# Kernel tuning notes

Measured on AMD Instinct MI355X. Metric: run time of the kernel, lower is better.

## Reference

```python
import jax, jax.numpy as jnp
import numpy as np

N, E, F, C = 50000, 640000, 128, 128  # nodes, edges, in_feat, hidden_channels
NEG_SLOPE = 0.2  # PyG GATConv default negative_slope


def setup_inputs() -> dict:
    key = jax.random.key(0)
    ks = jax.random.split(key, 16)
    s_in = 1.0 / np.sqrt(F)
    s_hid = 1.0 / np.sqrt(C)
    inp = {
        'x': jax.random.normal(ks[0], (N, F), jnp.float32),
        'edge_index': jax.random.randint(ks[1], (2, E), 0, N),
        # layer 1: GATConv (lin_src, lin_dst, att_src, att_dst, bias) + skip Linear
        'W1s': jax.random.normal(ks[2], (F, C), jnp.float32) * s_in,
        'W1d': jax.random.normal(ks[3], (F, C), jnp.float32) * s_in,
        'a1s': jax.random.normal(ks[4], (C,), jnp.float32) * s_hid,
        'a1d': jax.random.normal(ks[5], (C,), jnp.float32) * s_hid,
        'b1': jnp.zeros((C,), jnp.float32),
        'Wl1': jax.random.normal(ks[6], (F, C), jnp.float32) * s_in,
        'bl1': jnp.zeros((C,), jnp.float32),
        # layer 2
        'W2s': jax.random.normal(ks[7], (C, C), jnp.float32) * s_hid,
        'W2d': jax.random.normal(ks[8], (C, C), jnp.float32) * s_hid,
        'a2s': jax.random.normal(ks[9], (C,), jnp.float32) * s_hid,
        'a2d': jax.random.normal(ks[10], (C,), jnp.float32) * s_hid,
        'b2': jnp.zeros((C,), jnp.float32),
        'Wl2': jax.random.normal(ks[11], (C, C), jnp.float32) * s_hid,
        'bl2': jnp.zeros((C,), jnp.float32),
    }
    return inp


def gat_conv(x, Ws, Wd, a_s, a_d, b, src, dst):
    # project once per node, not per edge
    h_src = x @ Ws                      # [N, C]
    h_dst = x @ Wd                      # [N, C]
    alpha_src = h_src @ a_s             # [N]
    alpha_dst = h_dst @ a_d             # [N]
    # attention logits on edges: LeakyReLU(a_src[j] + a_dst[i]) for edge j->i
    e = jax.nn.leaky_relu(alpha_src[src] + alpha_dst[dst], NEG_SLOPE)  # [E]
    # segment softmax over incoming edges of each destination node
    e_max = jax.ops.segment_max(e, dst, num_segments=N)                # [N]
    e_exp = jnp.exp(e - e_max[dst])                                    # [E]
    e_sum = jax.ops.segment_sum(e_exp, dst, num_segments=N)            # [N]
    alpha = e_exp / (e_sum[dst] + 1e-16)                               # [E]
    # weighted message gather + scatter-add aggregation
    out = jax.ops.segment_sum(h_src[src] * alpha[:, None], dst, num_segments=N)  # [N, C]
    return out + b


def reference(x, edge_index, W1s, W1d, a1s, a1d, b1, Wl1, bl1,
              W2s, W2d, a2s, a2d, b2, Wl2, bl2):
    src, dst = edge_index[0], edge_index[1]
    h = gat_conv(x, W1s, W1d, a1s, a1d, b1, src, dst) + x @ Wl1 + bl1
    h = jax.nn.relu(h)
    out = gat_conv(h, W2s, W2d, a2s, a2d, b2, src, dst) + h @ Wl2 + bl2
    return out
```

## Files before the change

### kernel.cpp

```cpp
#include <hip/hip_runtime.h>


#define NEG_SLOPE 0.2f
#define SCAN_T 256
#define SCAN_ELE 1024

typedef __attribute__((ext_vector_type(8))) short short8;
typedef __attribute__((ext_vector_type(4))) float f32x4;

__device__ __forceinline__ unsigned short f2bf(float f) {
  unsigned u = __float_as_uint(f);
  u += 0x7FFF + ((u >> 16) & 1);
  return (unsigned short)(u >> 16);
}
__device__ __forceinline__ float bflo(unsigned v) { return __uint_as_float(v << 16); }
__device__ __forceinline__ float bfhi(unsigned v) { return __uint_as_float(v & 0xFFFF0000u); }

__global__ __launch_bounds__(256) void zero_kernel(int* __restrict__ p, int n) {
  int i = blockIdx.x * 256 + threadIdx.x;
  if (i < n) p[i] = 0;
}

__global__ __launch_bounds__(256) void count_kernel(const int* __restrict__ dst,
                                                    int* __restrict__ deg, int E) {
  int e = (blockIdx.x * 256 + threadIdx.x) * 2;
  if (e + 1 < E) {
    int2 d = *(const int2*)(dst + e);
    atomicAdd(&deg[d.x], 1);
    atomicAdd(&deg[d.y], 1);
  } else if (e < E) {
    atomicAdd(&deg[dst[e]], 1);
  }
}

__global__ __launch_bounds__(SCAN_T) void scan_pre(const int* __restrict__ deg,
                                                   int* __restrict__ bsum, int n) {
  __shared__ int red[SCAN_T];
  int b = blockIdx.x, t = threadIdx.x;
  int base = b * SCAN_ELE + t * 4;
  int s = 0;
#pragma unroll
  for (int j = 0; j < 4; ++j) {
    int i = base + j;
    if (i < n) s += deg[i];
  }
  red[t] = s;
  __syncthreads();
  for (int d = SCAN_T / 2; d > 0; d >>= 1) {
    if (t < d) red[t] += red[t + d];
    __syncthreads();
  }
  if (t == 0) bsum[b] = red[0];
}

__global__ __launch_bounds__(256) void scan_mid(const int* __restrict__ bsum,
                                                int* __restrict__ boff,
                                                int* __restrict__ off, int nb, int n) {
  __shared__ int sh[256];
  int t = threadIdx.x;
  int v = (t < nb) ? bsum[t] : 0;
  sh[t] = v;
  __syncthreads();
  for (int d = 1; d < 256; d <<= 1) {
    int u = (t >= d) ? sh[t - d] : 0;
    __syncthreads();
    sh[t] += u;
    __syncthreads();
  }
  if (t < nb) boff[t] = (t == 0) ? 0 : sh[t - 1];
  if (t == 255) off[n] = sh[255];
}

__global__ __launch_bounds__(SCAN_T) void scan_post(const int* __restrict__ deg,
                                                    const int* __restrict__ boff,
                                                    int* __restrict__ off,
                                                    int* __restrict__ cursor, int n) {
  __shared__ int tsum[SCAN_T];
  int b = blockIdx.x, t = threadIdx.x;
  int base = b * SCAN_ELE + t * 4;
  int v[4];
  int s = 0;
#pragma unroll
  for (int j = 0; j < 4; ++j) {
    int i = base + j;
    v[j] = (i < n) ? deg[i] : 0;
    s += v[j];
  }
  tsum[t] = s;
  __syncthreads();
  for (int d = 1; d < SCAN_T; d <<= 1) {
    int u = (t >= d) ? tsum[t - d] : 0;
    __syncthreads();
    tsum[t] += u;
    __syncthreads();
  }
  int run = boff[b] + ((t == 0) ? 0 : tsum[t - 1]);
#pragma unroll
  for (int j = 0; j < 4; ++j) {
    int i = base + j;
    if (i < n) {
      off[i] = run;
      cursor[i] = run;
      run += v[j];
    }
  }
}

__global__ __launch_bounds__(256) void scatter_kernel(const int* __restrict__ src,
                                                      const int* __restrict__ dst,
                                                      int* __restrict__ cursor,
                                                      int* __restrict__ ssorted, int E) {
  int e = (blockIdx.x * 256 + threadIdx.x) * 2;
  if (e + 1 < E) {
    int2 s = *(const int2*)(src + e);
    int2 d = *(const int2*)(dst + e);
    int p0 = atomicAdd(&cursor[d.x], 1);
    ssorted[p0] = s.x;
    int p1 = atomicAdd(&cursor[d.y], 1);
    ssorted[p1] = s.y;
  } else if (e < E) {
    int d = dst[e];
    int pos = atomicAdd(&cursor[d], 1);
    ssorted[pos] = src[e];
  }
}

__global__ __launch_bounds__(256) void wtrans_all(
    const float* __restrict__ W1s, const float* __restrict__ Wl1,
    const float* __restrict__ W2s, const float* __restrict__ Wl2,
    const float* __restrict__ a1s, const float* __restrict__ a1d,
    const float* __restrict__ a2s, const float* __restrict__ a2d,
    const float* __restrict__ W1d, const float* __restrict__ W2d,
    unsigned short* __restrict__ Wt, float* __restrict__ wv) {
  if (blockIdx.x < 256) {
    int idx = blockIdx.x * 256 + threadIdx.x;
    int which = idx >> 14;
    int j = idx & 16383;
    const float* W = (which == 0) ? W1s : (which == 1) ? Wl1 : (which == 2) ? W2s : Wl2;
    int k = j >> 7, c = j & 127;
    Wt[which * 16384 + c * 128 + k] = f2bf(W[k * 128 + c]);
  } else {
    for (int rep = 0; rep < 2; ++rep) {
      int item = threadIdx.x + rep * 256;
      int which = item >> 7, f = item & 127;
      const float* W;
      const float* a;
      if (which == 0)      { W = W1s; a = a1s; }
      else if (which == 1) { W = W1d; a = a1d; }
      else if (which == 2) { W = W2s; a = a2s; }
      else                 { W = W2d; a = a2d; }
      float s = 0.f;
#pragma unroll 8
      for (int c = 0; c < 128; ++c) s += W[f * 128 + c] * a[c];
      wv[which * 128 + f] = s;
    }
  }
}

__global__ __launch_bounds__(256) void prep1(const float* __restrict__ X,
                                             const float* __restrict__ wv,
                                             unsigned short* __restrict__ Xb,
                                             float* __restrict__ asrc,
                                             float* __restrict__ adst, int n) {
  int lane = threadIdx.x & 63;
  int wid = threadIdx.x >> 6;
  int node = blockIdx.x * 4 + wid;
  if (node >= n) return;
  float2 xv = ((const float2*)X)[(size_t)node * 64 + lane];
  float2 sv = ((const float2*)wv)[lane];
  float2 dv = ((const float2*)(wv + 128))[lane];
  unsigned pack = (unsigned)f2bf(xv.x) | ((unsigned)f2bf(xv.y) << 16);
  ((unsigned*)Xb)[(size_t)node * 64 + lane] = pack;
  float ds = xv.x * sv.x + xv.y * sv.y;
  float dd = xv.x * dv.x + xv.y * dv.y;
#pragma unroll
  for (int o = 32; o > 0; o >>= 1) {
    ds += __shfl_down(ds, o);
    dd += __shfl_down(dd, o);
  }
  if (lane == 0) {
    asrc[node] = ds;
    adst[node] = dd;
  }
}

#define SWZ(row, e) ((e) ^ (((row) & 7) << 3))

__global__ __launch_bounds__(256) void gemm_mfma(const unsigned short* __restrict__ Xb,
                                                 const unsigned short* __restrict__ WtA,
                                                 const unsigned short* __restrict__ WtB,
                                                 const float* __restrict__ biasb,
                                                 unsigned short* __restrict__ hsrc,
                                                 float* __restrict__ skip, int n) {
  __shared__ unsigned short sX[64 * 128];
  __shared__ unsigned short sW[128 * 128];
  int y = blockIdx.y;
  const unsigned short* Wt = (y == 0) ? WtA : WtB;
  int r0 = blockIdx.x * 64;
  int tid = threadIdx.x;

#pragma unroll
  for (int cch = 0; cch < 4; ++cch) {
    int id = tid + cch * 256;
    int r = id >> 4;
    int e = (id & 15) * 8;
    int gr = r0 + r;
    short8 v = (short8){0, 0, 0, 0, 0, 0, 0, 0};
    if (gr < n) v = *(const short8*)(Xb + (size_t)gr * 128 + e);
    *(short8*)&sX[r * 128 + SWZ(r, e)] = v;
  }
#pragma unroll
  for (int cch = 0; cch < 8; ++cch) {
    int id = tid + cch * 256;
    int r = id >> 4;
    int e = (id & 15) * 8;
    short8 v = *(const short8*)(Wt + r * 128 + e);
    *(short8*)&sW[r * 128 + SWZ(r, e)] = v;
  }
  __syncthreads();

  int w = tid >> 6, l = tid & 63;
  int q = l >> 4, fr = l & 15;
  int arow = w * 16 + fr;

  short8 af[4];
#pragma unroll
  for (int ks = 0; ks < 4; ++ks)
    af[ks] = *(short8*)&sX[arow * 128 + SWZ(arow, ks * 32 + q * 8)];

  f32x4 acc[8];
#pragma unroll
  for (int ct = 0; ct < 8; ++ct) acc[ct] = (f32x4){0.f, 0.f, 0.f, 0.f};

#pragma unroll
  for (int ct = 0; ct < 8; ++ct) {
    int brow = ct * 16 + fr;
#pragma unroll
    for (int ks = 0; ks < 4; ++ks) {
      short8 bf = *(short8*)&sW[brow * 128 + SWZ(brow, ks * 32 + q * 8)];
      acc[ct] = __builtin_amdgcn_mfma_f32_16x16x32_bf16(af[ks], bf, acc[ct], 0, 0, 0);
    }
  }

  if (y == 0) {
#pragma unroll
    for (int ct = 0; ct < 8; ++ct) {
#pragma unroll
      for (int i = 0; i < 4; ++i) {
        int grow = r0 + w * 16 + q * 4 + i;
        if (grow < n) hsrc[(size_t)grow * 128 + ct * 16 + fr] = f2bf(acc[ct][i]);
      }
    }
  } else {
#pragma unroll
    for (int ct = 0; ct < 8; ++ct) {
      float bv = biasb[ct * 16 + fr];
#pragma unroll
      for (int i = 0; i < 4; ++i) {
        int grow = r0 + w * 16 + q * 4 + i;
        if (grow < n) skip[(size_t)grow * 128 + ct * 16 + fr] = acc[ct][i] + bv;
      }
    }
  }
}

__global__ __launch_bounds__(256) void agg_fused(const int* __restrict__ off,
                                                 const int* __restrict__ ssorted,
                                                 const float* __restrict__ asrc,
                                                 const float* __restrict__ adst,
                                                 const unsigned short* __restrict__ hs,
                                                 const float* __restrict__ skip,
                                                 const float* __restrict__ bias,
                                                 float* __restrict__ outp,
                                                 unsigned short* __restrict__ xb,
                                                 const float* __restrict__ wv2,
                                                 float* __restrict__ asrc2,
                                                 float* __restrict__ adst2,
                                                 int relu, int n) {
  __shared__ float2 s_ae[4][66];
  int lane = threadIdx.x & 63;
  int wid = threadIdx.x >> 6;
  int i = blockIdx.x * 4 + wid;
  if (i >= n) return;
  int s0 = off[i], s1 = off[i + 1];
  float ad = adst[i];
  int half = lane >> 5;
  int cl = lane & 31;

  float a0x = 0.f, a0y = 0.f, a0z = 0.f, a0w = 0.f;
  float a1x = 0.f, a1y = 0.f, a1z = 0.f, a1w = 0.f;
  float psum = 0.f;
  for (int cb = s0; cb < s1; cb += 64) {
    int m = min(64, s1 - cb);
    if (lane < m) {
      int sv = ssorted[cb + lane];
      float e = asrc[sv] + ad;
      e = (e > 0.f) ? e : NEG_SLOPE * e;
      float a = __expf(e);
      psum += a;
      s_ae[wid][lane] = make_float2(a, __int_as_float(sv));
    }
    if (lane == 0 && (m & 1)) s_ae[wid][m] = make_float2(0.f, __int_as_float(0));
    int npair = (m + 1) >> 1;
    int t = 0;
    for (; t + 2 <= npair; t += 2) {
      float2 p0 = s_ae[wid][2 * t + half];
      float2 p1 = s_ae[wid][2 * t + 2 + half];
      uint2 v0 = *(const uint2*)(hs + (size_t)__float_as_int(p0.y) * 128 + cl * 4);
      uint2 v1 = *(const uint2*)(hs + (size_t)__float_as_int(p1.y) * 128 + cl * 4);
      a0x += p0.x * bflo(v0.x); a0y += p0.x * bfhi(v0.x);
      a0z += p0.x * bflo(v0.y); a0w += p0.x * bfhi(v0.y);
      a1x += p1.x * bflo(v1.x); a1y += p1.x * bfhi(v1.x);
      a1z += p1.x * bflo(v1.y); a1w += p1.x * bfhi(v1.y);
    }
    if (t < npair) {
      float2 p0 = s_ae[wid][2 * t + half];
      uint2 v0 = *(const uint2*)(hs + (size_t)__float_as_int(p0.y) * 128 + cl * 4);
      a0x += p0.x * bflo(v0.x); a0y += p0.x * bfhi(v0.x);
      a0z += p0.x * bflo(v0.y); a0w += p0.x * bfhi(v0.y);
    }
  }
#pragma unroll
  for (int o = 32; o > 0; o >>= 1) psum += __shfl_xor(psum, o);
  float inv = 1.f / (psum + 1e-16f);

  float cx = a0x + a1x, cy = a0y + a1y, cz = a0z + a1z, cw = a0w + a1w;
  cx += __shfl_xor(cx, 32);
  cy += __shfl_xor(cy, 32);
  cz += __shfl_xor(cz, 32);
  cw += __shfl_xor(cw, 32);

  float v0 = 0.f, v1 = 0.f, v2 = 0.f, v3 = 0.f;
  if (half == 0) {
    float4 sk = ((const float4*)skip)[(size_t)i * 32 + cl];
    float4 bv = ((const float4*)bias)[cl];
    v0 = cx * inv + bv.x + sk.x;
    v1 = cy * inv + bv.y + sk.y;
    v2 = cz * inv + bv.z + sk.z;
    v3 = cw * inv + bv.w + sk.w;
    if (relu) {
      v0 = fmaxf(v0, 0.f); v1 = fmaxf(v1, 0.f);
      v2 = fmaxf(v2, 0.f); v3 = fmaxf(v3, 0.f);
    }
    if (outp) {
      float4 vo; vo.x = v0; vo.y = v1; vo.z = v2; vo.w = v3;
      ((float4*)outp)[(size_t)i * 32 + cl] = vo;
    }
    if (xb) {
      uint2 pack;
      pack.x = (unsigned)f2bf(v0) | ((unsigned)f2bf(v1) << 16);
      pack.y = (unsigned)f2bf(v2) | ((unsigned)f2bf(v3) << 16);
      ((uint2*)xb)[(size_t)i * 32 + cl] = pack;
    }
  }
  if (xb) {
    float ds = 0.f, dd = 0.f;
    if (half == 0) {
      float4 sv2 = ((const float4*)wv2)[cl];
      float4 dv2 = ((const float4*)(wv2 + 128))[cl];
      ds = v0 * sv2.x + v1 * sv2.y + v2 * sv2.z + v3 * sv2.w;
      dd = v0 * dv2.x + v1 * dv2.y + v2 * dv2.z + v3 * dv2.w;
    }
#pragma unroll
    for (int o = 32; o > 0; o >>= 1) {
      ds += __shfl_xor(ds, o);
      dd += __shfl_xor(dd, o);
    }
    if (lane == 0) {
      asrc2[i] = ds;
      adst2[i] = dd;
    }
  }
}

extern "C" void kernel_launch(void* const* d_in, const int* in_sizes, int n_in,
                              void* d_out, int out_size, void* d_ws, size_t ws_size,
                              hipStream_t stream) {
  const float* x   = (const float*)d_in[0];
  const int*   ei  = (const int*)d_in[1];
  const float* W1s = (const float*)d_in[2];
  const float* W1d = (const float*)d_in[3];
  const float* a1s = (const float*)d_in[4];
  const float* a1d = (const float*)d_in[5];
  const float* b1  = (const float*)d_in[6];
  const float* Wl1 = (const float*)d_in[7];
  const float* bl1 = (const float*)d_in[8];
  const float* W2s = (const float*)d_in[9];
  const float* W2d = (const float*)d_in[10];
  const float* a2s = (const float*)d_in[11];
  const float* a2d = (const float*)d_in[12];
  const float* b2  = (const float*)d_in[13];
  const float* Wl2 = (const float*)d_in[14];
  const float* bl2 = (const float*)d_in[15];

  const int N = in_sizes[0] / 128;
  const int E = in_sizes[1] / 2;
  const int* srcp = ei;
  const int* dstp = ei + E;

  char* base = (char*)d_ws;
  size_t o = 0;
  auto alloc = [&](size_t bytes) -> void* {
    void* p = base + o;
    o += (bytes + 255) & ~(size_t)255;
    return p;
  };
  const int NB = (N + SCAN_ELE - 1) / SCAN_ELE;
  int*   deg     = (int*)alloc((size_t)N * 4);
  int*   off     = (int*)alloc((size_t)(N + 1) * 4);
  int*   cursor  = (int*)alloc((size_t)N * 4);
  int*   bsum    = (int*)alloc((size_t)NB * 4);
  int*   boff    = (int*)alloc((size_t)NB * 4);
  int*   ssorted = (int*)alloc((size_t)E * 4);
  float* asrcA   = (float*)alloc((size_t)N * 4);
  float* adstA   = (float*)alloc((size_t)N * 4);
  float* asrcB   = (float*)alloc((size_t)N * 4);
  float* adstB   = (float*)alloc((size_t)N * 4);
  float* wv      = (float*)alloc(4 * 128 * 4);
  unsigned short* Xb    = (unsigned short*)alloc((size_t)N * 128 * 2);
  unsigned short* Wt    = (unsigned short*)alloc(4 * 128 * 128 * 2);
  unsigned short* hsrcB = (unsigned short*)alloc((size_t)N * 128 * 2);
  float* skip    = (float*)alloc((size_t)N * 128 * 4);
  (void)ws_size; (void)n_in; (void)out_size;

  zero_kernel<<<(N + 255) / 256, 256, 0, stream>>>(deg, N);
  count_kernel<<<(E / 2 + 255) / 256, 256, 0, stream>>>(dstp, deg, E);
  scan_pre<<<NB, SCAN_T, 0, stream>>>(deg, bsum, N);
  scan_mid<<<1, 256, 0, stream>>>(bsum, boff, off, NB, N);
  scan_post<<<NB, SCAN_T, 0, stream>>>(deg, boff, off, cursor, N);
  scatter_kernel<<<(E / 2 + 255) / 256, 256, 0, stream>>>(srcp, dstp, cursor, ssorted, E);
  wtrans_all<<<257, 256, 0, stream>>>(W1s, Wl1, W2s, Wl2, a1s, a1d, a2s, a2d,
                                      W1d, W2d, Wt, wv);

  dim3 ggrid((N + 63) / 64, 2);
  int nwb = (N + 3) / 4;

  prep1<<<nwb, 256, 0, stream>>>(x, wv, Xb, asrcA, adstA, N);
  gemm_mfma<<<ggrid, 256, 0, stream>>>(Xb, Wt, Wt + 16384, bl1, hsrcB, skip, N);
  agg_fused<<<nwb, 256, 0, stream>>>(off, ssorted, asrcA, adstA, hsrcB, skip, b1,
                                     nullptr, Xb, wv + 256, asrcB, adstB, 1, N);

  gemm_mfma<<<ggrid, 256, 0, stream>>>(Xb, Wt + 2 * 16384, Wt + 3 * 16384, bl2,
                                       hsrcB, skip, N);
  agg_fused<<<nwb, 256, 0, stream>>>(off, ssorted, asrcB, adstB, hsrcB, skip, b2,
                                     (float*)d_out, nullptr, nullptr, nullptr,
                                     nullptr, 0, N);
}
```

Baseline: 316.0 us.

## Fuse input prep into GEMM and compute both projections per block

Removes the prep1 kernel. The layer-1 GEMM now reads fp32 x directly, converts it to bf16 in-kernel and computes the attention dot products with shuffles. The GEMM grid drops its y-dimension, so each block reuses its loaded X tile for both the source and skip projections, reloading the weight tile in between. The edge count and scatter kernels process four edges per thread with int4 loads, and the weight transpose swaps its k/c index mapping so writes are contiguous. Fewer blocks in the GEMM grid lowers parallelism, and the second weight load adds an extra barrier.

Result: faster. 307.1 us (-2.8%).

```diff
diff --git a/kernel.cpp b/kernel.cpp
--- a/kernel.cpp
+++ b/kernel.cpp
@@ -23,13 +23,15 @@
 
 __global__ __launch_bounds__(256) void count_kernel(const int* __restrict__ dst,
                                                     int* __restrict__ deg, int E) {
-  int e = (blockIdx.x * 256 + threadIdx.x) * 2;
-  if (e + 1 < E) {
-    int2 d = *(const int2*)(dst + e);
+  int e = (blockIdx.x * 256 + threadIdx.x) * 4;
+  if (e + 3 < E) {
+    int4 d = *(const int4*)(dst + e);
     atomicAdd(&deg[d.x], 1);
     atomicAdd(&deg[d.y], 1);
-  } else if (e < E) {
-    atomicAdd(&deg[dst[e]], 1);
+    atomicAdd(&deg[d.z], 1);
+    atomicAdd(&deg[d.w], 1);
+  } else {
+    for (int k = e; k < E; ++k) atomicAdd(&deg[dst[k]], 1);
   }
 }
 
@@ -110,18 +112,16 @@
                                                       const int* __restrict__ dst,
                                                       int* __restrict__ cursor,
                                                       int* __restrict__ ssorted, int E) {
-  int e = (blockIdx.x * 256 + threadIdx.x) * 2;
-  if (e + 1 < E) {
-    int2 s = *(const int2*)(src + e);
-    int2 d = *(const int2*)(dst + e);
-    int p0 = atomicAdd(&cursor[d.x], 1);
-    ssorted[p0] = s.x;
-    int p1 = atomicAdd(&cursor[d.y], 1);
-    ssorted[p1] = s.y;
-  } else if (e < E) {
-    int d = dst[e];
-    int pos = atomicAdd(&cursor[d], 1);
-    ssorted[pos] = src[e];
+  int e = (blockIdx.x * 256 + threadIdx.x) * 4;
+  if (e + 3 < E) {
+    int4 s = *(const int4*)(src + e);
+    int4 d = *(const int4*)(dst + e);
+    ssorted[atomicAdd(&cursor[d.x], 1)] = s.x;
+    ssorted[atomicAdd(&cursor[d.y], 1)] = s.y;
+    ssorted[atomicAdd(&cursor[d.z], 1)] = s.z;
+    ssorted[atomicAdd(&cursor[d.w], 1)] = s.w;
+  } else {
+    for (int k = e; k < E; ++k) ssorted[atomicAdd(&cursor[dst[k]], 1)] = src[k];
   }
 }
 
@@ -137,7 +137,7 @@
     int which = idx >> 14;
     int j = idx & 16383;
     const float* W = (which == 0) ? W1s : (which == 1) ? Wl1 : (which == 2) ? W2s : Wl2;
-    int k = j >> 7, c = j & 127;
+    int c = j >> 7, k = j & 127;
     Wt[which * 16384 + c * 128 + k] = f2bf(W[k * 128 + c]);
   } else {
     for (int rep = 0; rep < 2; ++rep) {
@@ -157,45 +157,17 @@
   }
 }
 
-__global__ __launch_bounds__(256) void prep1(const float* __restrict__ X,
-                                             const float* __restrict__ wv,
-                                             unsigned short* __restrict__ Xb,
-                                             float* __restrict__ asrc,
-                                             float* __restrict__ adst, int n) {
-  int lane = threadIdx.x & 63;
-  int wid = threadIdx.x >> 6;
-  int node = blockIdx.x * 4 + wid;
-  if (node >= n) return;
-  float2 xv = ((const float2*)X)[(size_t)node * 64 + lane];
-  float2 sv = ((const float2*)wv)[lane];
-  float2 dv = ((const float2*)(wv + 128))[lane];
-  unsigned pack = (unsigned)f2bf(xv.x) | ((unsigned)f2bf(xv.y) << 16);
-  ((unsigned*)Xb)[(size_t)node * 64 + lane] = pack;
-  float ds = xv.x * sv.x + xv.y * sv.y;
-  float dd = xv.x * dv.x + xv.y * dv.y;
-#pragma unroll
-  for (int o = 32; o > 0; o >>= 1) {
-    ds += __shfl_down(ds, o);
-    dd += __shfl_down(dd, o);
-  }
-  if (lane == 0) {
-    asrc[node] = ds;
-    adst[node] = dd;
-  }
-}
-
 #define SWZ(row, e) ((e) ^ (((row) & 7) << 3))
 
-__global__ __launch_bounds__(256) void gemm_mfma(const unsigned short* __restrict__ Xb,
-                                                 const unsigned short* __restrict__ WtA,
-                                                 const unsigned short* __restrict__ WtB,
-                                                 const float* __restrict__ biasb,
-                                                 unsigned short* __restrict__ hsrc,
-                                                 float* __restrict__ skip, int n) {
+template <int L1>
+__global__ __launch_bounds__(256) void gemm_mfma(
+    const void* __restrict__ srcX, const unsigned short* __restrict__ WtA,
+    const unsigned short* __restrict__ WtB, const float* __restrict__ biasb,
+    const float* __restrict__ wvsd, unsigned short* __restrict__ hsrc,
+    float* __restrict__ skip, float* __restrict__ asrc, float* __restrict__ adst,
+    int n) {
   __shared__ unsigned short sX[64 * 128];
   __shared__ unsigned short sW[128 * 128];
-  int y = blockIdx.y;
-  const unsigned short* Wt = (y == 0) ? WtA : WtB;
   int r0 = blockIdx.x * 64;
   int tid = threadIdx.x;
 
@@ -203,19 +175,51 @@
   for (int cch = 0; cch < 4; ++cch) {
     int id = tid + cch * 256;
     int r = id >> 4;
-    int e = (id & 15) * 8;
+    int e8 = (id & 15) * 8;
     int gr = r0 + r;
     short8 v = (short8){0, 0, 0, 0, 0, 0, 0, 0};
-    if (gr < n) v = *(const short8*)(Xb + (size_t)gr * 128 + e);
-    *(short8*)&sX[r * 128 + SWZ(r, e)] = v;
-  }
+    float ds = 0.f, dd = 0.f;
+    if (gr < n) {
+      if (L1) {
+        const float* xr = (const float*)srcX + (size_t)gr * 128 + e8;
+        float4 f0 = *(const float4*)xr;
+        float4 f1 = *(const float4*)(xr + 4);
+        v[0] = (short)f2bf(f0.x); v[1] = (short)f2bf(f0.y);
+        v[2] = (short)f2bf(f0.z); v[3] = (short)f2bf(f0.w);
+        v[4] = (short)f2bf(f1.x); v[5] = (short)f2bf(f1.y);
+        v[6] = (short)f2bf(f1.z); v[7] = (short)f2bf(f1.w);
+        float4 s0 = *(const float4*)(wvsd + e8);
+        float4 s1 = *(const float4*)(wvsd + e8 + 4);
+        float4 d0 = *(const float4*)(wvsd + 128 + e8);
+        float4 d1 = *(const float4*)(wvsd + 128 + e8 + 4);
+        ds = f0.x * s0.x + f0.y * s0.y + f0.z * s0.z + f0.w * s0.w +
+             f1.x * s1.x + f1.y * s1.y + f1.z * s1.z + f1.w * s1.w;
+        dd = f0.x * d0.x + f0.y * d0.y + f0.z * d0.z + f0.w * d0.w +
+             f1.x * d1.x + f1.y * d1.y + f1.z * d1.z + f1.w * d1.w;
+      } else {
+        v = *(const short8*)((const unsigned short*)srcX + (size_t)gr * 128 + e8);
+      }
+    }
+    *(short8*)&sX[r * 128 + SWZ(r, e8)] = v;
+    if (L1) {
+#pragma unroll
+      for (int o = 8; o > 0; o >>= 1) {
+        ds += __shfl_down(ds, o);
+        dd += __shfl_down(dd, o);
+      }
+      if ((tid & 15) == 0 && gr < n) {
+        asrc[gr] = ds;
+        adst[gr] = dd;
+      }
+    }
+  }
+
 #pragma unroll
   for (int cch = 0; cch < 8; ++cch) {
     int id = tid + cch * 256;
-    int r = id >> 4;
-    int e = (id & 15) * 8;
-    short8 v = *(const short8*)(Wt + r * 128 + e);
-    *(short8*)&sW[r * 128 + SWZ(r, e)] = v;
+    int rr = id >> 4;
+    int ee = (id & 15) * 8;
+    *(short8*)&sW[rr * 128 + SWZ(rr, ee)] = *(const short8*)(WtA + rr * 128 + ee);
   }
   __syncthreads();
 
@@ -231,7 +235,6 @@
   f32x4 acc[8];
 #pragma unroll
   for (int ct = 0; ct < 8; ++ct) acc[ct] = (f32x4){0.f, 0.f, 0.f, 0.f};
-
 #pragma unroll
   for (int ct = 0; ct < 8; ++ct) {
     int brow = ct * 16 + fr;
@@ -241,25 +244,43 @@
       acc[ct] = __builtin_amdgcn_mfma_f32_16x16x32_bf16(af[ks], bf, acc[ct], 0, 0, 0);
     }
   }
-
-  if (y == 0) {
-#pragma unroll
-    for (int ct = 0; ct < 8; ++ct) {
-#pragma unroll
-      for (int i = 0; i < 4; ++i) {
-        int grow = r0 + w * 16 + q * 4 + i;
-        if (grow < n) hsrc[(size_t)grow * 128 + ct * 16 + fr] = f2bf(acc[ct][i]);
-      }
-    }
-  } else {
-#pragma unroll
-    for (int ct = 0; ct < 8; ++ct) {
-      float bv = biasb[ct * 16 + fr];
-#pragma unroll
-      for (int i = 0; i < 4; ++i) {
-        int grow = r0 + w * 16 + q * 4 + i;
-        if (grow < n) skip[(size_t)grow * 128 + ct * 16 + fr] = acc[ct][i] + bv;
-      }
+#pragma unroll
+  for (int ct = 0; ct < 8; ++ct) {
+#pragma unroll
+    for (int i = 0; i < 4; ++i) {
+      int grow = r0 + w * 16 + q * 4 + i;
+      if (grow < n) hsrc[(size_t)grow * 128 + ct * 16 + fr] = f2bf(acc[ct][i]);
+    }
+  }
+  __syncthreads();
+
+#pragma unroll
+  for (int cch = 0; cch < 8; ++cch) {
+    int id = tid + cch * 256;
+    int rr = id >> 4;
+    int ee = (id & 15) * 8;
+    *(short8*)&sW[rr * 128 + SWZ(rr, ee)] = *(const short8*)(WtB + rr * 128 + ee);
+  }
+  __syncthreads();
+
+#pragma unroll
+  for (int ct = 0; ct < 8; ++ct) acc[ct] = (f32x4){0.f, 0.f, 0.f, 0.f};
+#pragma unroll
+  for (int ct = 0; ct < 8; ++ct) {
+    int brow = ct * 16 + fr;
+#pragma unroll
+    for (int ks = 0; ks < 4; ++ks) {
+      short8 bf = *(short8*)&sW[brow * 128 + SWZ(brow, ks * 32 + q * 8)];
+      acc[ct] = __builtin_amdgcn_mfma_f32_16x16x32_bf16(af[ks], bf, acc[ct], 0, 0, 0);
+    }
+  }
+#pragma unroll
+  for (int ct = 0; ct < 8; ++ct) {
+    float bv = biasb[ct * 16 + fr];
+#pragma unroll
+    for (int i = 0; i < 4; ++i) {
+      int grow = r0 + w * 16 + q * 4 + i;
+      if (grow < n) skip[(size_t)grow * 128 + ct * 16 + fr] = acc[ct][i] + bv;
     }
   }
 }
@@ -424,24 +445,24 @@
   (void)ws_size; (void)n_in; (void)out_size;
 
   zero_kernel<<<(N + 255) / 256, 256, 0, stream>>>(deg, N);
-  count_kernel<<<(E / 2 + 255) / 256, 256, 0, stream>>>(dstp, deg, E);
+  count_kernel<<<(E / 4 + 255) / 256, 256, 0, stream>>>(dstp, deg, E);
   scan_pre<<<NB, SCAN_T, 0, stream>>>(deg, bsum, N);
   scan_mid<<<1, 256, 0, stream>>>(bsum, boff, off, NB, N);
   scan_post<<<NB, SCAN_T, 0, stream>>>(deg, boff, off, cursor, N);
-  scatter_kernel<<<(E / 2 + 255) / 256, 256, 0, stream>>>(srcp, dstp, cursor, ssorted, E);
+  scatter_kernel<<<(E / 4 + 255) / 256, 256, 0, stream>>>(srcp, dstp, cursor, ssorted, E);
   wtrans_all<<<257, 256, 0, stream>>>(W1s, Wl1, W2s, Wl2, a1s, a1d, a2s, a2d,
                                       W1d, W2d, Wt, wv);
 
-  dim3 ggrid((N + 63) / 64, 2);
+  int ggrid = (N + 63) / 64;
   int nwb = (N + 3) / 4;
 
-  prep1<<<nwb, 256, 0, stream>>>(x, wv, Xb, asrcA, adstA, N);
-  gemm_mfma<<<ggrid, 256, 0, stream>>>(Xb, Wt, Wt + 16384, bl1, hsrcB, skip, N);
+  gemm_mfma<1><<<ggrid, 256, 0, stream>>>(x, Wt, Wt + 16384, bl1, wv, hsrcB,
+                                          skip, asrcA, adstA, N);
   agg_fused<<<nwb, 256, 0, stream>>>(off, ssorted, asrcA, adstA, hsrcB, skip, b1,
                                      nullptr, Xb, wv + 256, asrcB, adstB, 1, N);
 
-  gemm_mfma<<<ggrid, 256, 0, stream>>>(Xb, Wt + 2 * 16384, Wt + 3 * 16384, bl2,
-                                       hsrcB, skip, N);
+  gemm_mfma<0><<<ggrid, 256, 0, stream>>>(Xb, Wt + 2 * 16384, Wt + 3 * 16384, bl2,
+                                          nullptr, hsrcB, skip, nullptr, nullptr, N);
   agg_fused<<<nwb, 256, 0, stream>>>(off, ssorted, asrcB, adstB, hsrcB, skip, b2,
                                      (float*)d_out, nullptr, nullptr, nullptr,
                                      nullptr, 0, N);
```
